# Optimization experiments

Hardware: AMD Instinct MI355X
Metric: run time of the kernel (lower is better)

Reference implementation:

```python
import jax, jax.numpy as jnp
import numpy as np

H = 128  # hidden_dim
D = 128  # input_dim


def _lstm_scan(x_seq, Wih, Whh, bih, bhh, reverse=False):
    """x_seq: [T,B,Din]; returns h outputs [T,B,H] in original time order.
    PyTorch LSTMCell gate order: i, f, g, o."""
    hdim = Whh.shape[1]
    B = x_seq.shape[1]
    # Precompute input projections for all timesteps in one GEMM.
    xg = jnp.einsum('tbd,gd->tbg', x_seq, Wih) + bih  # [T,B,4H]

    def step(carry, xg_t):
        h, c = carry
        gates = xg_t + h @ Whh.T + bhh
        i, f, g, o = jnp.split(gates, 4, axis=-1)
        i = jax.nn.sigmoid(i)
        f = jax.nn.sigmoid(f)
        g = jnp.tanh(g)
        o = jax.nn.sigmoid(o)
        c = f * c + i * g
        h = o * jnp.tanh(c)
        return (h, c), h

    h0 = jnp.zeros((B, hdim), dtype=x_seq.dtype)
    c0 = jnp.zeros((B, hdim), dtype=x_seq.dtype)
    _, hs = jax.lax.scan(step, (h0, c0), xg, reverse=reverse)
    return hs  # [T,B,H], original time order (scan reverse handles bw dir)


def _bilstm_layer(x_seq, params_fw, params_bw):
    fw = _lstm_scan(x_seq, *params_fw, reverse=False)
    bw = _lstm_scan(x_seq, *params_bw, reverse=True)
    return jnp.concatenate([fw, bw], axis=-1)  # [T,B,2H]


def _make_cell_params(key, in_dim, hid):
    k1, k2, k3, k4 = jax.random.split(key, 4)
    s = 1.0 / np.sqrt(hid)
    return (
        jax.random.uniform(k1, (4 * hid, in_dim), jnp.float32, -s, s),
        jax.random.uniform(k2, (4 * hid, hid), jnp.float32, -s, s),
        jax.random.uniform(k3, (4 * hid,), jnp.float32, -s, s),
        jax.random.uniform(k4, (4 * hid,), jnp.float32, -s, s),
    )


def setup_inputs() -> dict:
    key = jax.random.key(0)
    ks = jax.random.split(key, 6)
    B, T = 64, 1024
    x = jax.random.normal(ks[0], (B, T, D), jnp.float32)
    lengths = jax.random.randint(ks[1], (B,), 1, T + 1, jnp.int64 if jax.config.jax_enable_x64 else jnp.int32)
    inp = {'x': x, 'lengths': lengths}
    names = ['fw1', 'bw1', 'fw2', 'bw2']
    in_dims = [D, D, 2 * H, 2 * H]
    for name, idim, k in zip(names, in_dims, ks[2:]):
        Wih, Whh, bih, bhh = _make_cell_params(k, idim, H)
        inp[f'Wih_{name}'] = Wih
        inp[f'Whh_{name}'] = Whh
        inp[f'bih_{name}'] = bih
        inp[f'bhh_{name}'] = bhh
    return inp


def reference(x, lengths,
              Wih_fw1, Whh_fw1, bih_fw1, bhh_fw1,
              Wih_bw1, Whh_bw1, bih_bw1, bhh_bw1,
              Wih_fw2, Whh_fw2, bih_fw2, bhh_fw2,
              Wih_bw2, Whh_bw2, bih_bw2, bhh_bw2):
    # lengths is unused in the original forward as well.
    xt = jnp.transpose(x, (1, 0, 2))  # [T,B,D] time-major for scan
    out1 = _bilstm_layer(xt,
                         (Wih_fw1, Whh_fw1, bih_fw1, bhh_fw1),
                         (Wih_bw1, Whh_bw1, bih_bw1, bhh_bw1))
    out2 = _bilstm_layer(out1,
                         (Wih_fw2, Whh_fw2, bih_fw2, bhh_fw2),
                         (Wih_bw2, Whh_bw2, bih_bw2, bhh_bw2))
    return jnp.transpose(out2, (1, 0, 2))  # [B,T,2H]
```

## Files before the change

kernel.cpp:

```cpp
#include <hip/hip_runtime.h>
#include <hip/hip_fp16.h>
#include <stdint.h>


#define T_SEQ 1024
#define B_SZ  64
#define M_TOT 65536

typedef _Float16 h2_t __attribute__((ext_vector_type(2)));
typedef _Float16 f16x8 __attribute__((ext_vector_type(8)));
typedef float f32x4 __attribute__((ext_vector_type(4)));

__device__ inline uint32_t pack2(float a, float b) {
  uint16_t ua = __builtin_bit_cast(uint16_t, (_Float16)a);
  uint16_t ub = __builtin_bit_cast(uint16_t, (_Float16)b);
  return (uint32_t)ua | ((uint32_t)ub << 16);
}

template <int CTRL>
__device__ inline float dppf(float v) {
  return __builtin_bit_cast(
      float, __builtin_amdgcn_update_dpp(0, __builtin_bit_cast(int, v), CTRL,
                                         0xF, 0xF, true));
}


__global__ void prep_whB(const float* __restrict__ Whh, uint32_t* __restrict__ dst) {
  int idx = blockIdx.x * 256 + threadIdx.x;
  int gp = idx >> 6, kw = idx & 63;
  int g = ((gp & 3) << 7) | (gp >> 2);
  dst[idx] = pack2(Whh[g * 128 + 2 * kw], Whh[g * 128 + 2 * kw + 1]);
}

template <int KW>
__global__ void prep_bt(const float* __restrict__ Wih, uint32_t* __restrict__ dst) {
  int idx = blockIdx.x * 256 + threadIdx.x;
  constexpr int SH = (KW == 64) ? 6 : 7;
  int g = idx >> SH, kw = idx & (KW - 1);
  dst[idx] = pack2(Wih[g * (2 * KW) + 2 * kw], Wih[g * (2 * KW) + 2 * kw + 1]);
}

__global__ void prep_biasc(const float* __restrict__ bih, const float* __restrict__ bhh,
                           float* __restrict__ dst) {
  int idx = blockIdx.x * 256 + threadIdx.x;
  if (idx < 512) dst[idx] = bih[idx] + bhh[idx];
}

__global__ void prep_x(const float2* __restrict__ x2, uint32_t* __restrict__ xf16) {
  int idx = blockIdx.x * 256 + threadIdx.x;
  float2 v = x2[idx];
  xf16[idx] = pack2(v.x, v.y);
}

template <int KW>
__global__ __launch_bounds__(256) void xg_gemm(
    const uint32_t* __restrict__ A, const uint32_t* __restrict__ Bt,
    const float* __restrict__ biascat, uint16_t* __restrict__ xg) {
  const int n0 = blockIdx.x * 64;
  const int m0 = blockIdx.y * 64;
  const int tid = threadIdx.x;
  __shared__ uint32_t At[64][36];
  __shared__ uint32_t Bts[64][36];
  const int lr = tid >> 2, lq = tid & 3;
  const int wave = tid >> 6, lane = tid & 63;
  const int wm = wave >> 1, wn = wave & 1;
  const int q = lane >> 4, ln16 = lane & 15;
  f32x4 acc[2][2] = {};
  for (int kb = 0; kb < KW; kb += 16) {
    uint4 av = *(const uint4*)&A[(size_t)(m0 + lr) * KW + kb + lq * 4];
    uint4 bv = *(const uint4*)&Bt[(size_t)(n0 + lr) * KW + kb + lq * 4];
    __syncthreads();
    *(uint4*)&At[lr][lq * 4] = av;
    *(uint4*)&Bts[lr][lq * 4] = bv;
    __syncthreads();
#pragma unroll
    for (int mi = 0; mi < 2; mi++) {
      f16x8 af = *(const f16x8*)&At[wm * 32 + mi * 16 + ln16][q * 4];
#pragma unroll
      for (int ni = 0; ni < 2; ni++) {
        f16x8 bf = *(const f16x8*)&Bts[wn * 32 + ni * 16 + ln16][q * 4];
        acc[mi][ni] = __builtin_amdgcn_mfma_f32_16x16x32_f16(af, bf, acc[mi][ni], 0, 0, 0);
      }
    }
  }
#pragma unroll
  for (int mi = 0; mi < 2; mi++)
#pragma unroll
    for (int ni = 0; ni < 2; ni++) {
      int n = n0 + wn * 32 + ni * 16 + ln16;
      int cell = n >> 9, g = n & 511;
      int gp = ((g & 127) << 2) | (g >> 7);
      float bs = biascat[n];
#pragma unroll
      for (int i = 0; i < 4; i++) {
        int m = m0 + wm * 32 + mi * 16 + q * 4 + i;
        float v = acc[mi][ni][i] + bs;
        xg[((size_t)cell * M_TOT + m) * 512 + gp] =
            __builtin_bit_cast(uint16_t, (_Float16)v);
      }
    }
}

template <bool FINAL>
__global__ __launch_bounds__(512, 2) void scan_kernel(
    const uint16_t* __restrict__ xg, const uint32_t* __restrict__ whB,
    uint16_t* __restrict__ hout, float* __restrict__ fout) {
  const int tid = threadIdx.x;
  const int j = tid >> 2;
  const int p = tid & 3;
  const int w = tid >> 6;
  const int lane = tid & 63;
  const int q = lane >> 4;
  const int ln16 = lane & 15;
  const int b = blockIdx.x & 63;
  const int dir = blockIdx.x >> 6;

  __shared__ __align__(16) uint32_t hbuf[2][64];

  f16x8 wb[4][4];
  {
    const uint32_t* wp = whB + (size_t)dir * 512 * 64;
#pragma unroll
    for (int nt = 0; nt < 4; nt++)
#pragma unroll
      for (int kt = 0; kt < 4; kt++)
        wb[nt][kt] = *(const f16x8*)&wp[(64 * w + 16 * nt + ln16) * 64 + 16 * kt + q * 4];
  }
#pragma unroll
  for (int nt = 0; nt < 4; nt++)
#pragma unroll
    for (int kt = 0; kt < 4; kt++) asm volatile("" : "+v"(wb[nt][kt]));

  const float kmul = (p == 2) ? (-2.0f * 1.44269504f) : -1.44269504f;
  const float gm = (p == 2) ? 2.0f : 1.0f;
  const float gb = (p == 2) ? -1.0f : 0.0f;

  const uint16_t* xgp = xg + ((size_t)dir * M_TOT + b * T_SEQ) * 512 + tid;

  if (tid < 64) hbuf[0][tid] = 0u;
  float c = 0.0f;
  const f32x4 zero4 = {0.0f, 0.0f, 0.0f, 0.0f};

  uint16_t xr[8];
#pragma unroll
  for (int k = 0; k < 4; k++) {
    const int tk = dir ? (T_SEQ - 1 - k) : k;
    xr[k] = xgp[(size_t)tk * 512];
  }
  __syncthreads();

  for (int s0 = 0; s0 < T_SEQ; s0 += 8) {
#pragma unroll
    for (int nt = 0; nt < 4; nt++)
#pragma unroll
      for (int kt = 0; kt < 4; kt++) asm volatile("" : "+v"(wb[nt][kt]));
#pragma unroll
    for (int k = 0; k < 8; k++) {
      const int s = s0 + k;
      const int par = k & 1;

      {
        int sn = s + 4;
        sn = (sn < T_SEQ) ? sn : (T_SEQ - 1);
        const int tn = dir ? (T_SEQ - 1 - sn) : sn;
        xr[(k + 4) & 7] = xgp[(size_t)tn * 512];
      }

      const uint4* hb4 = (const uint4*)&hbuf[par][0];
      f32x4 a0 = zero4, a1 = zero4, a2 = zero4, a3 = zero4;
#pragma unroll
      for (int kt = 0; kt < 4; kt++) {
        f16x8 hk = __builtin_bit_cast(f16x8, hb4[kt * 4 + q]);
        a0 = __builtin_amdgcn_mfma_f32_16x16x32_f16(hk, wb[0][kt], a0, 0, 0, 0);
        a1 = __builtin_amdgcn_mfma_f32_16x16x32_f16(hk, wb[1][kt], a1, 0, 0, 0);
        a2 = __builtin_amdgcn_mfma_f32_16x16x32_f16(hk, wb[2][kt], a2, 0, 0, 0);
        a3 = __builtin_amdgcn_mfma_f32_16x16x32_f16(hk, wb[3][kt], a3, 0, 0, 0);
      }
      float zs = (q & 2) ? ((q & 1) ? a3[0] : a2[0]) : ((q & 1) ? a1[0] : a0[0]);

      float z = zs + (float)__builtin_bit_cast(_Float16, xr[k]);

      float e = __builtin_amdgcn_exp2f(z * kmul);
      float sg = __builtin_amdgcn_rcpf(1.0f + e);
      float gv = __builtin_fmaf(sg, gm, gb);

      float gi = dppf<0x00>(gv);
      float gf = dppf<0x55>(gv);
      float gg = dppf<0xAA>(gv);
      float go = dppf<0xFF>(gv);

      c = __builtin_fmaf(gf, c, gi * gg);
      float ec = __builtin_amdgcn_exp2f(c * (-2.0f * 1.44269504f));
      float th = __builtin_fmaf(2.0f, __builtin_amdgcn_rcpf(1.0f + ec), -1.0f);
      float h = go * th;

      if (p == 0) {
        const int t = dir ? (T_SEQ - 1 - s) : s;
        uint16_t hu = __builtin_bit_cast(uint16_t, (_Float16)h);
        ((uint16_t*)(&hbuf[par ^ 1][0]))[j] = hu;
        if (FINAL) {
          fout[(size_t)(b * T_SEQ + t) * 256 + dir * 128 + j] = h;
        } else {
          hout[(size_t)(b * T_SEQ + t) * 256 + dir * 128 + j] = hu;
        }
      }
      asm volatile("s_waitcnt lgkmcnt(0)" ::: "memory");
      __builtin_amdgcn_s_barrier();
      asm volatile("" ::: "memory");
    }
  }
}

extern "C" void kernel_launch(void* const* d_in, const int* in_sizes, int n_in,
                              void* d_out, int out_size, void* d_ws, size_t ws_size,
                              hipStream_t stream) {
  const float* x = (const float*)d_in[0];
  const float* Wih_fw1 = (const float*)d_in[2];
  const float* Whh_fw1 = (const float*)d_in[3];
  const float* bih_fw1 = (const float*)d_in[4];
  const float* bhh_fw1 = (const float*)d_in[5];
  const float* Wih_bw1 = (const float*)d_in[6];
  const float* Whh_bw1 = (const float*)d_in[7];
  const float* bih_bw1 = (const float*)d_in[8];
  const float* bhh_bw1 = (const float*)d_in[9];
  const float* Wih_fw2 = (const float*)d_in[10];
  const float* Whh_fw2 = (const float*)d_in[11];
  const float* bih_fw2 = (const float*)d_in[12];
  const float* bhh_fw2 = (const float*)d_in[13];
  const float* Wih_bw2 = (const float*)d_in[14];
  const float* Whh_bw2 = (const float*)d_in[15];
  const float* bih_bw2 = (const float*)d_in[16];
  const float* bhh_bw2 = (const float*)d_in[17];

  uint8_t* ws = (uint8_t*)d_ws;
  uint32_t* whbuf = (uint32_t*)(ws + 0);
  uint32_t* btbuf1 = (uint32_t*)(ws + 524288);
  uint32_t* btbuf2 = (uint32_t*)(ws + 786432);
  float* biascat = (float*)(ws + 1310720);
  uint32_t* xf16 = (uint32_t*)(ws + 2097152);
  uint32_t* out1 = (uint32_t*)(ws + 18874368);
  uint16_t* xgbuf = (uint16_t*)(ws + 52428800);
  float* fout = (float*)d_out;

  prep_whB<<<128, 256, 0, stream>>>(Whh_fw1, whbuf + 0 * 32768);
  prep_whB<<<128, 256, 0, stream>>>(Whh_bw1, whbuf + 1 * 32768);
  prep_whB<<<128, 256, 0, stream>>>(Whh_fw2, whbuf + 2 * 32768);
  prep_whB<<<128, 256, 0, stream>>>(Whh_bw2, whbuf + 3 * 32768);
  prep_bt<64><<<128, 256, 0, stream>>>(Wih_fw1, btbuf1 + 0);
  prep_bt<64><<<128, 256, 0, stream>>>(Wih_bw1, btbuf1 + 512 * 64);
  prep_bt<128><<<256, 256, 0, stream>>>(Wih_fw2, btbuf2 + 0);
  prep_bt<128><<<256, 256, 0, stream>>>(Wih_bw2, btbuf2 + 512 * 128);
  prep_biasc<<<2, 256, 0, stream>>>(bih_fw1, bhh_fw1, biascat + 0);
  prep_biasc<<<2, 256, 0, stream>>>(bih_bw1, bhh_bw1, biascat + 512);
  prep_biasc<<<2, 256, 0, stream>>>(bih_fw2, bhh_fw2, biascat + 1024);
  prep_biasc<<<2, 256, 0, stream>>>(bih_bw2, bhh_bw2, biascat + 1536);
  prep_x<<<(B_SZ * T_SEQ * 64) / 256, 256, 0, stream>>>((const float2*)x, xf16);

  xg_gemm<64><<<dim3(16, 1024), 256, 0, stream>>>(xf16, btbuf1, biascat, xgbuf);
  scan_kernel<false><<<128, 512, 0, stream>>>(xgbuf, whbuf + 0, (uint16_t*)out1, nullptr);

  xg_gemm<128><<<dim3(16, 1024), 256, 0, stream>>>(out1, btbuf2, biascat + 1024, xgbuf);
  scan_kernel<true><<<128, 512, 0, stream>>>(xgbuf, whbuf + 2 * 32768, nullptr, fout);
}
```

Before: 1.304 ms.

## Halve scan block to 4 waves with each thread computing two hidden units

The recurrent scan kernel moves from 512 to 256 threads per block. Each wave now holds twice as many Whh MFMA tiles (8 n-tiles) and each thread evaluates the gates for two hidden units, with h written as packed half2 pairs. The Whh prep layout and the xg GEMM output permutation are reworked to match, so each thread loads one 32-bit xg word per step. The aim is fewer waves taking part in the per-timestep barrier, which shortens the serial critical path, at the cost of more MFMA work and register pressure per wave.

```diff
diff --git a/kernel.cpp b/kernel.cpp
--- a/kernel.cpp
+++ b/kernel.cpp
@@ -27,8 +27,10 @@
 
 __global__ void prep_whB(const float* __restrict__ Whh, uint32_t* __restrict__ dst) {
   int idx = blockIdx.x * 256 + threadIdx.x;
-  int gp = idx >> 6, kw = idx & 63;
-  int g = ((gp & 3) << 7) | (gp >> 2);
+  int R = idx >> 6, kw = idx & 63;
+  int w = R >> 7, nt = (R >> 4) & 7, cc = R & 15;
+  int j = 32 * w + 8 * (nt >> 1) + 2 * (cc >> 2) + (nt & 1);
+  int g = (cc & 3) * 128 + j;
   dst[idx] = pack2(Whh[g * 128 + 2 * kw], Whh[g * 128 + 2 * kw + 1]);
 }
 
@@ -89,45 +91,47 @@
     for (int ni = 0; ni < 2; ni++) {
       int n = n0 + wn * 32 + ni * 16 + ln16;
       int cell = n >> 9, g = n & 511;
-      int gp = ((g & 127) << 2) | (g >> 7);
+      int j = g & 127, pg = g >> 7;
+      int PI = ((j >> 5) << 7) | (((j >> 3) & 3) << 5) | (((j >> 1) & 3) << 3) |
+               (pg << 1) | (j & 1);
       float bs = biascat[n];
 #pragma unroll
       for (int i = 0; i < 4; i++) {
         int m = m0 + wm * 32 + mi * 16 + q * 4 + i;
         float v = acc[mi][ni][i] + bs;
-        xg[((size_t)cell * M_TOT + m) * 512 + gp] =
+        xg[((size_t)cell * M_TOT + m) * 512 + PI] =
             __builtin_bit_cast(uint16_t, (_Float16)v);
       }
     }
 }
 
 template <bool FINAL>
-__global__ __launch_bounds__(512, 2) void scan_kernel(
+__global__ __launch_bounds__(256, 1) void scan_kernel(
     const uint16_t* __restrict__ xg, const uint32_t* __restrict__ whB,
-    uint16_t* __restrict__ hout, float* __restrict__ fout) {
+    uint32_t* __restrict__ hout, float* __restrict__ fout) {
   const int tid = threadIdx.x;
-  const int j = tid >> 2;
-  const int p = tid & 3;
   const int w = tid >> 6;
   const int lane = tid & 63;
   const int q = lane >> 4;
   const int ln16 = lane & 15;
+  const int mq = ln16 >> 2;
+  const int p = ln16 & 3;
   const int b = blockIdx.x & 63;
   const int dir = blockIdx.x >> 6;
 
   __shared__ __align__(16) uint32_t hbuf[2][64];
 
-  f16x8 wb[4][4];
+  f16x8 wb[8][4];
   {
     const uint32_t* wp = whB + (size_t)dir * 512 * 64;
 #pragma unroll
-    for (int nt = 0; nt < 4; nt++)
+    for (int nt = 0; nt < 8; nt++)
 #pragma unroll
       for (int kt = 0; kt < 4; kt++)
-        wb[nt][kt] = *(const f16x8*)&wp[(64 * w + 16 * nt + ln16) * 64 + 16 * kt + q * 4];
-  }
-#pragma unroll
-  for (int nt = 0; nt < 4; nt++)
+        wb[nt][kt] = *(const f16x8*)&wp[(128 * w + 16 * nt + ln16) * 64 + 16 * kt + 4 * q];
+  }
+#pragma unroll
+  for (int nt = 0; nt < 8; nt++)
 #pragma unroll
     for (int kt = 0; kt < 4; kt++) asm volatile("" : "+v"(wb[nt][kt]));
 
@@ -135,23 +139,23 @@
   const float gm = (p == 2) ? 2.0f : 1.0f;
   const float gb = (p == 2) ? -1.0f : 0.0f;
 
-  const uint16_t* xgp = xg + ((size_t)dir * M_TOT + b * T_SEQ) * 512 + tid;
+  const uint32_t* xgp = (const uint32_t*)xg + ((size_t)dir * M_TOT + (size_t)b * T_SEQ) * 256 + tid;
 
   if (tid < 64) hbuf[0][tid] = 0u;
-  float c = 0.0f;
+  float c0 = 0.0f, c1 = 0.0f;
   const f32x4 zero4 = {0.0f, 0.0f, 0.0f, 0.0f};
 
-  uint16_t xr[8];
+  uint32_t xr[8];
 #pragma unroll
   for (int k = 0; k < 4; k++) {
     const int tk = dir ? (T_SEQ - 1 - k) : k;
-    xr[k] = xgp[(size_t)tk * 512];
+    xr[k] = xgp[(size_t)tk * 256];
   }
   __syncthreads();
 
   for (int s0 = 0; s0 < T_SEQ; s0 += 8) {
 #pragma unroll
-    for (int nt = 0; nt < 4; nt++)
+    for (int nt = 0; nt < 8; nt++)
 #pragma unroll
       for (int kt = 0; kt < 4; kt++) asm volatile("" : "+v"(wb[nt][kt]));
 #pragma unroll
@@ -163,45 +167,65 @@
         int sn = s + 4;
         sn = (sn < T_SEQ) ? sn : (T_SEQ - 1);
         const int tn = dir ? (T_SEQ - 1 - sn) : sn;
-        xr[(k + 4) & 7] = xgp[(size_t)tn * 512];
+        xr[(k + 4) & 7] = xgp[(size_t)tn * 256];
       }
 
       const uint4* hb4 = (const uint4*)&hbuf[par][0];
-      f32x4 a0 = zero4, a1 = zero4, a2 = zero4, a3 = zero4;
-#pragma unroll
-      for (int kt = 0; kt < 4; kt++) {
+      f32x4 acc[8];
+      {
+        f16x8 hk = __builtin_bit_cast(f16x8, hb4[q]);
+#pragma unroll
+        for (int nt = 0; nt < 8; nt++)
+          acc[nt] = __builtin_amdgcn_mfma_f32_16x16x32_f16(hk, wb[nt][0], zero4, 0, 0, 0);
+      }
+#pragma unroll
+      for (int kt = 1; kt < 4; kt++) {
         f16x8 hk = __builtin_bit_cast(f16x8, hb4[kt * 4 + q]);
-        a0 = __builtin_amdgcn_mfma_f32_16x16x32_f16(hk, wb[0][kt], a0, 0, 0, 0);
-        a1 = __builtin_amdgcn_mfma_f32_16x16x32_f16(hk, wb[1][kt], a1, 0, 0, 0);
-        a2 = __builtin_amdgcn_mfma_f32_16x16x32_f16(hk, wb[2][kt], a2, 0, 0, 0);
-        a3 = __builtin_amdgcn_mfma_f32_16x16x32_f16(hk, wb[3][kt], a3, 0, 0, 0);
-      }
-      float zs = (q & 2) ? ((q & 1) ? a3[0] : a2[0]) : ((q & 1) ? a1[0] : a0[0]);
-
-      float z = zs + (float)__builtin_bit_cast(_Float16, xr[k]);
-
-      float e = __builtin_amdgcn_exp2f(z * kmul);
-      float sg = __builtin_amdgcn_rcpf(1.0f + e);
-      float gv = __builtin_fmaf(sg, gm, gb);
-
-      float gi = dppf<0x00>(gv);
-      float gf = dppf<0x55>(gv);
-      float gg = dppf<0xAA>(gv);
-      float go = dppf<0xFF>(gv);
-
-      c = __builtin_fmaf(gf, c, gi * gg);
-      float ec = __builtin_amdgcn_exp2f(c * (-2.0f * 1.44269504f));
-      float th = __builtin_fmaf(2.0f, __builtin_amdgcn_rcpf(1.0f + ec), -1.0f);
-      float h = go * th;
+#pragma unroll
+        for (int nt = 0; nt < 8; nt++)
+          acc[nt] = __builtin_amdgcn_mfma_f32_16x16x32_f16(hk, wb[nt][kt], acc[nt], 0, 0, 0);
+      }
+
+      float z0 = (q & 2) ? ((q & 1) ? acc[6][0] : acc[4][0])
+                         : ((q & 1) ? acc[2][0] : acc[0][0]);
+      float z1 = (q & 2) ? ((q & 1) ? acc[7][0] : acc[5][0])
+                         : ((q & 1) ? acc[3][0] : acc[1][0]);
+
+      h2_t xv = __builtin_bit_cast(h2_t, xr[k]);
+      z0 += (float)xv[0];
+      z1 += (float)xv[1];
+
+      float e0 = __builtin_amdgcn_exp2f(z0 * kmul);
+      float e1 = __builtin_amdgcn_exp2f(z1 * kmul);
+      float sg0 = __builtin_amdgcn_rcpf(1.0f + e0);
+      float sg1 = __builtin_amdgcn_rcpf(1.0f + e1);
+      float gv0 = __builtin_fmaf(sg0, gm, gb);
+      float gv1 = __builtin_fmaf(sg1, gm, gb);
+
+      float gi0 = dppf<0x00>(gv0), gf0 = dppf<0x55>(gv0);
+      float gg0 = dppf<0xAA>(gv0), go0 = dppf<0xFF>(gv0);
+      float gi1 = dppf<0x00>(gv1), gf1 = dppf<0x55>(gv1);
+      float gg1 = dppf<0xAA>(gv1), go1 = dppf<0xFF>(gv1);
+
+      c0 = __builtin_fmaf(gf0, c0, gi0 * gg0);
+      c1 = __builtin_fmaf(gf1, c1, gi1 * gg1);
+      float ec0 = __builtin_amdgcn_exp2f(c0 * (-2.0f * 1.44269504f));
+      float ec1 = __builtin_amdgcn_exp2f(c1 * (-2.0f * 1.44269504f));
+      float th0 = __builtin_fmaf(2.0f, __builtin_amdgcn_rcpf(1.0f + ec0), -1.0f);
+      float th1 = __builtin_fmaf(2.0f, __builtin_amdgcn_rcpf(1.0f + ec1), -1.0f);
+      float h0 = go0 * th0;
+      float h1 = go1 * th1;
 
       if (p == 0) {
+        const int uo = 16 * w + 4 * q + mq;
+        uint32_t hu = pack2(h0, h1);
+        hbuf[par ^ 1][uo] = hu;
         const int t = dir ? (T_SEQ - 1 - s) : s;
-        uint16_t hu = __builtin_bit_cast(uint16_t, (_Float16)h);
-        ((uint16_t*)(&hbuf[par ^ 1][0]))[j] = hu;
         if (FINAL) {
-          fout[(size_t)(b * T_SEQ + t) * 256 + dir * 128 + j] = h;
+          float2 hv = {h0, h1};
+          ((float2*)fout)[(size_t)(b * T_SEQ + t) * 128 + dir * 64 + uo] = hv;
         } else {
-          hout[(size_t)(b * T_SEQ + t) * 256 + dir * 128 + j] = hu;
+          hout[(size_t)(b * T_SEQ + t) * 128 + dir * 64 + uo] = hu;
         }
       }
       asm volatile("s_waitcnt lgkmcnt(0)" ::: "memory");
@@ -257,8 +281,8 @@
   prep_x<<<(B_SZ * T_SEQ * 64) / 256, 256, 0, stream>>>((const float2*)x, xf16);
 
   xg_gemm<64><<<dim3(16, 1024), 256, 0, stream>>>(xf16, btbuf1, biascat, xgbuf);
-  scan_kernel<false><<<128, 512, 0, stream>>>(xgbuf, whbuf + 0, (uint16_t*)out1, nullptr);
+  scan_kernel<false><<<128, 256, 0, stream>>>(xgbuf, whbuf + 0, out1, nullptr);
 
   xg_gemm<128><<<dim3(16, 1024), 256, 0, stream>>>(out1, btbuf2, biascat + 1024, xgbuf);
-  scan_kernel<true><<<128, 512, 0, stream>>>(xgbuf, whbuf + 2 * 32768, nullptr, fout);
-}
+  scan_kernel<true><<<128, 256, 0, stream>>>(xgbuf, whbuf + 2 * 32768, nullptr, fout);
+}
```

New measurement: 1.327 ms. About the same (+1.8%).

## Fuse weight prep into one kernel and pre-permute Wih rows for contiguous xg stores

Applied to the files above, without the earlier changes.

Merges the twelve small weight and bias prep launches into a single fused kernel. The gate interleave permutation moves from the GEMM epilogue into the Wih/bias prep, so the xg GEMM writes consecutive columns to consecutive addresses instead of scattering them with a stride of 4. The scan loop also drops the clamp on the xg prefetch index and starts the first MFMA from a zero accumulator. Without the clamp, the prefetch reads past the sequence bounds (discarded values), which could touch memory outside the buffer for edge batches.

```diff
diff --git a/kernel.cpp b/kernel.cpp
--- a/kernel.cpp
+++ b/kernel.cpp
@@ -24,26 +24,48 @@
                                          0xF, 0xF, true));
 }
 
-
-__global__ void prep_whB(const float* __restrict__ Whh, uint32_t* __restrict__ dst) {
-  int idx = blockIdx.x * 256 + threadIdx.x;
-  int gp = idx >> 6, kw = idx & 63;
-  int g = ((gp & 3) << 7) | (gp >> 2);
-  dst[idx] = pack2(Whh[g * 128 + 2 * kw], Whh[g * 128 + 2 * kw + 1]);
-}
-
-template <int KW>
-__global__ void prep_bt(const float* __restrict__ Wih, uint32_t* __restrict__ dst) {
-  int idx = blockIdx.x * 256 + threadIdx.x;
-  constexpr int SH = (KW == 64) ? 6 : 7;
-  int g = idx >> SH, kw = idx & (KW - 1);
-  dst[idx] = pack2(Wih[g * (2 * KW) + 2 * kw], Wih[g * (2 * KW) + 2 * kw + 1]);
-}
-
-__global__ void prep_biasc(const float* __restrict__ bih, const float* __restrict__ bhh,
-                           float* __restrict__ dst) {
-  int idx = blockIdx.x * 256 + threadIdx.x;
-  if (idx < 512) dst[idx] = bih[idx] + bhh[idx];
+__global__ void fused_prep(
+    const float* __restrict__ Whh0, const float* __restrict__ Whh1,
+    const float* __restrict__ Whh2, const float* __restrict__ Whh3,
+    const float* __restrict__ Wih0, const float* __restrict__ Wih1,
+    const float* __restrict__ Wih2, const float* __restrict__ Wih3,
+    const float* __restrict__ bih0, const float* __restrict__ bih1,
+    const float* __restrict__ bih2, const float* __restrict__ bih3,
+    const float* __restrict__ bhh0, const float* __restrict__ bhh1,
+    const float* __restrict__ bhh2, const float* __restrict__ bhh3,
+    uint32_t* __restrict__ whbuf, uint32_t* __restrict__ btbuf1,
+    uint32_t* __restrict__ btbuf2, float* __restrict__ biascat) {
+  const int blk = blockIdx.x;
+  const int tid = threadIdx.x;
+  if (blk < 512) {
+    int e = blk * 256 + tid;
+    int c = e >> 15, e2 = e & 32767;
+    const float* W = (c == 0) ? Whh0 : (c == 1) ? Whh1 : (c == 2) ? Whh2 : Whh3;
+    int R = e2 >> 6, kw = e2 & 63;
+    int g = ((R & 3) << 7) | (R >> 2);
+    whbuf[c * 32768 + e2] = pack2(W[g * 128 + 2 * kw], W[g * 128 + 2 * kw + 1]);
+  } else if (blk < 768) {
+    int e = (blk - 512) * 256 + tid;
+    int c = e >> 15, e2 = e & 32767;
+    const float* W = c ? Wih1 : Wih0;
+    int r = e2 >> 6, kw = e2 & 63;
+    int g = ((r & 3) << 7) | (r >> 2);
+    btbuf1[c * 32768 + e2] = pack2(W[g * 128 + 2 * kw], W[g * 128 + 2 * kw + 1]);
+  } else if (blk < 1280) {
+    int e = (blk - 768) * 256 + tid;
+    int c = e >> 16, e2 = e & 65535;
+    const float* W = c ? Wih3 : Wih2;
+    int r = e2 >> 7, kw = e2 & 127;
+    int g = ((r & 3) << 7) | (r >> 2);
+    btbuf2[c * 65536 + e2] = pack2(W[g * 256 + 2 * kw], W[g * 256 + 2 * kw + 1]);
+  } else {
+    int e = (blk - 1280) * 256 + tid;
+    int lc = e >> 9, gp = e & 511;
+    const float* bi = (lc == 0) ? bih0 : (lc == 1) ? bih1 : (lc == 2) ? bih2 : bih3;
+    const float* bh = (lc == 0) ? bhh0 : (lc == 1) ? bhh1 : (lc == 2) ? bhh2 : bhh3;
+    int g = ((gp & 3) << 7) | (gp >> 2);
+    biascat[e] = bi[g] + bh[g];
+  }
 }
 
 __global__ void prep_x(const float2* __restrict__ x2, uint32_t* __restrict__ xf16) {
@@ -88,8 +110,7 @@
 #pragma unroll
     for (int ni = 0; ni < 2; ni++) {
       int n = n0 + wn * 32 + ni * 16 + ln16;
-      int cell = n >> 9, g = n & 511;
-      int gp = ((g & 127) << 2) | (g >> 7);
+      int cell = n >> 9, gp = n & 511;
       float bs = biascat[n];
 #pragma unroll
       for (int i = 0; i < 4; i++) {
@@ -124,7 +145,7 @@
     for (int nt = 0; nt < 4; nt++)
 #pragma unroll
       for (int kt = 0; kt < 4; kt++)
-        wb[nt][kt] = *(const f16x8*)&wp[(64 * w + 16 * nt + ln16) * 64 + 16 * kt + q * 4];
+        wb[nt][kt] = *(const f16x8*)&wp[(64 * w + 16 * nt + ln16) * 64 + 16 * kt + 4 * q];
   }
 #pragma unroll
   for (int nt = 0; nt < 4; nt++)
@@ -135,7 +156,7 @@
   const float gm = (p == 2) ? 2.0f : 1.0f;
   const float gb = (p == 2) ? -1.0f : 0.0f;
 
-  const uint16_t* xgp = xg + ((size_t)dir * M_TOT + b * T_SEQ) * 512 + tid;
+  const uint16_t* xgp = xg + ((size_t)dir * M_TOT + (size_t)b * T_SEQ) * 512 + tid;
 
   if (tid < 64) hbuf[0][tid] = 0u;
   float c = 0.0f;
@@ -160,16 +181,21 @@
       const int par = k & 1;
 
       {
-        int sn = s + 4;
-        sn = (sn < T_SEQ) ? sn : (T_SEQ - 1);
-        const int tn = dir ? (T_SEQ - 1 - sn) : sn;
-        xr[(k + 4) & 7] = xgp[(size_t)tn * 512];
+        const int tn = dir ? (T_SEQ - 1 - (s + 4)) : (s + 4);
+        xr[(k + 4) & 7] = *(xgp + (ptrdiff_t)tn * 512);
       }
 
       const uint4* hb4 = (const uint4*)&hbuf[par][0];
-      f32x4 a0 = zero4, a1 = zero4, a2 = zero4, a3 = zero4;
-#pragma unroll
-      for (int kt = 0; kt < 4; kt++) {
+      f32x4 a0, a1, a2, a3;
+      {
+        f16x8 hk = __builtin_bit_cast(f16x8, hb4[q]);
+        a0 = __builtin_amdgcn_mfma_f32_16x16x32_f16(hk, wb[0][0], zero4, 0, 0, 0);
+        a1 = __builtin_amdgcn_mfma_f32_16x16x32_f16(hk, wb[1][0], zero4, 0, 0, 0);
+        a2 = __builtin_amdgcn_mfma_f32_16x16x32_f16(hk, wb[2][0], zero4, 0, 0, 0);
+        a3 = __builtin_amdgcn_mfma_f32_16x16x32_f16(hk, wb[3][0], zero4, 0, 0, 0);
+      }
+#pragma unroll
+      for (int kt = 1; kt < 4; kt++) {
         f16x8 hk = __builtin_bit_cast(f16x8, hb4[kt * 4 + q]);
         a0 = __builtin_amdgcn_mfma_f32_16x16x32_f16(hk, wb[0][kt], a0, 0, 0, 0);
         a1 = __builtin_amdgcn_mfma_f32_16x16x32_f16(hk, wb[1][kt], a1, 0, 0, 0);
@@ -238,27 +264,22 @@
   uint32_t* btbuf2 = (uint32_t*)(ws + 786432);
   float* biascat = (float*)(ws + 1310720);
   uint32_t* xf16 = (uint32_t*)(ws + 2097152);
-  uint32_t* out1 = (uint32_t*)(ws + 18874368);
+  uint16_t* out1 = (uint16_t*)(ws + 18874368);
   uint16_t* xgbuf = (uint16_t*)(ws + 52428800);
   float* fout = (float*)d_out;
 
-  prep_whB<<<128, 256, 0, stream>>>(Whh_fw1, whbuf + 0 * 32768);
-  prep_whB<<<128, 256, 0, stream>>>(Whh_bw1, whbuf + 1 * 32768);
-  prep_whB<<<128, 256, 0, stream>>>(Whh_fw2, whbuf + 2 * 32768);
-  prep_whB<<<128, 256, 0, stream>>>(Whh_bw2, whbuf + 3 * 32768);
-  prep_bt<64><<<128, 256, 0, stream>>>(Wih_fw1, btbuf1 + 0);
-  prep_bt<64><<<128, 256, 0, stream>>>(Wih_bw1, btbuf1 + 512 * 64);
-  prep_bt<128><<<256, 256, 0, stream>>>(Wih_fw2, btbuf2 + 0);
-  prep_bt<128><<<256, 256, 0, stream>>>(Wih_bw2, btbuf2 + 512 * 128);
-  prep_biasc<<<2, 256, 0, stream>>>(bih_fw1, bhh_fw1, biascat + 0);
-  prep_biasc<<<2, 256, 0, stream>>>(bih_bw1, bhh_bw1, biascat + 512);
-  prep_biasc<<<2, 256, 0, stream>>>(bih_fw2, bhh_fw2, biascat + 1024);
-  prep_biasc<<<2, 256, 0, stream>>>(bih_bw2, bhh_bw2, biascat + 1536);
+  fused_prep<<<1288, 256, 0, stream>>>(
+      Whh_fw1, Whh_bw1, Whh_fw2, Whh_bw2,
+      Wih_fw1, Wih_bw1, Wih_fw2, Wih_bw2,
+      bih_fw1, bih_bw1, bih_fw2, bih_bw2,
+      bhh_fw1, bhh_bw1, bhh_fw2, bhh_bw2,
+      whbuf, btbuf1, btbuf2, biascat);
   prep_x<<<(B_SZ * T_SEQ * 64) / 256, 256, 0, stream>>>((const float2*)x, xf16);
 
   xg_gemm<64><<<dim3(16, 1024), 256, 0, stream>>>(xf16, btbuf1, biascat, xgbuf);
-  scan_kernel<false><<<128, 512, 0, stream>>>(xgbuf, whbuf + 0, (uint16_t*)out1, nullptr);
-
-  xg_gemm<128><<<dim3(16, 1024), 256, 0, stream>>>(out1, btbuf2, biascat + 1024, xgbuf);
+  scan_kernel<false><<<128, 512, 0, stream>>>(xgbuf, whbuf + 0, out1, nullptr);
+
+  xg_gemm<128><<<dim3(16, 1024), 256, 0, stream>>>((const uint32_t*)out1, btbuf2,
+                                                   biascat + 1024, xgbuf);
   scan_kernel<true><<<128, 512, 0, stream>>>(xgbuf, whbuf + 2 * 32768, nullptr, fout);
 }
```

Result: faster. 1.139 ms (-12.6%).
